# Kernel tuning notes

Hardware: AMD Instinct MI355X
Metric: run time of the kernel (lower is better)

Reference implementation:

```python
import jax, jax.numpy as jnp
import numpy as np

H = 512; W = 512; C = 32; B = 2; N = 120000; HEADS = 2; HD = C // HEADS; S = 9
INDEX_SHIFT = jnp.array([[0,0],[-1,0],[1,0],[0,1],[-1,1],[1,1],[0,-1],[-1,-1],[1,-1]], dtype=jnp.int32)


def setup_inputs() -> dict:
    key = jax.random.key(0)
    ks = jax.random.split(key, 20)
    bev_feats = jax.random.normal(ks[0], (B, N, C), jnp.float32)
    coors = []
    for b in range(B):
        perm = jax.random.permutation(ks[1 + b], H * W)[:N]
        coors.append(jnp.stack([perm // W, perm % W], axis=-1))
    bev_coors = jnp.stack(coors).astype(jnp.int32)
    s = 1.0 / np.sqrt(C)
    u = lambda k, shape, lim: jax.random.uniform(k, shape, jnp.float32, -lim, lim)
    return {
        'bev_feats': bev_feats,
        'bev_coors': bev_coors,
        'ln_w': jnp.ones((C,), jnp.float32),
        'ln_b': jnp.zeros((C,), jnp.float32),
        'wq': u(ks[3], (C, C), s), 'bq': u(ks[4], (C,), s),
        'wk': u(ks[5], (C, C), s), 'bk': u(ks[6], (C,), s),
        'wv': u(ks[7], (C, C), s), 'bv': u(ks[8], (C,), s),
        'pos_w': u(ks[9], (C, 2), 1.0 / np.sqrt(2.0)), 'pos_b': u(ks[10], (C,), 1.0 / np.sqrt(2.0)),
        'in_w': u(ks[11], (3 * C, C), s), 'in_b': jnp.zeros((3 * C,), jnp.float32),
        'out_w': u(ks[12], (C, C), s), 'out_b': jnp.zeros((C,), jnp.float32),
    }


def reference(bev_feats, bev_coors, ln_w, ln_b, wq, bq, wk, bk, wv, bv, pos_w, pos_b, in_w, in_b, out_w, out_b):
    def single(feats, coors):
        # LayerNorm (biased var, eps=1e-5)
        mu = feats.mean(-1, keepdims=True)
        var = feats.var(-1, keepdims=True)
        x = (feats - mu) / jnp.sqrt(var + 1e-5) * ln_w + ln_b
        # qkv 1x1 conv == linear
        q = x @ wq.T + bq
        k = x @ wk.T + bk
        v = x @ wv.T + bv
        # dense grid lookup: coord -> voxel index (-1 if empty)
        flat0 = coors[:, 0] * W + coors[:, 1]
        grid = jnp.full((H * W,), -1, jnp.int32).at[flat0].set(jnp.arange(N, dtype=jnp.int32))
        sc = coors[None] + INDEX_SHIFT[:, None]                      # [9,N,2]
        valid = (sc[..., 0] >= 0) & (sc[..., 0] < H) & (sc[..., 1] >= 0) & (sc[..., 1] < W)
        flat = jnp.clip(sc[..., 0], 0, H - 1) * W + jnp.clip(sc[..., 1], 0, W - 1)
        idx = jnp.where(valid, grid[flat], -1)                       # [9,N]
        pos = INDEX_SHIFT.astype(x.dtype) @ pos_w.T + pos_b          # [9,C]
        m = (idx >= 0)[..., None]
        tv = jnp.where(m, v[idx] + pos[:, None, :], 0.0)             # [9,N,C]
        tk = jnp.where(m, k[idx], 0.0)
        keyt = jnp.swapaxes(tk, 0, 1)                                # [N,9,C]
        valt = jnp.swapaxes(tv, 0, 1)
        # tiny MHA: query len 1, kv len 9, 2 heads (dropout inactive at eval)
        qp = q @ in_w[:C].T + in_b[:C]
        kp = keyt @ in_w[C:2 * C].T + in_b[C:2 * C]
        vp = valt @ in_w[2 * C:].T + in_b[2 * C:]
        qh = qp.reshape(N, HEADS, HD)
        kh = kp.reshape(N, S, HEADS, HD)
        vh = vp.reshape(N, S, HEADS, HD)
        attn = jax.nn.softmax(jnp.einsum('nhd,nshd->nhs', qh, kh) / np.sqrt(HD), axis=-1)
        o = jnp.einsum('nhs,nshd->nhd', attn, vh).reshape(N, C)
        o = o @ out_w.T + out_b
        # scatter to pseudo image [C,H,W]
        canvas = jnp.zeros((C, H * W), o.dtype).at[:, flat0].set(o.T)
        return canvas.reshape(C, H, W)
    return jax.vmap(single)(bev_feats, bev_coors)
```

## Files before the change

kernel.cpp:

```cpp
#include <hip/hip_runtime.h>
#include <hip/hip_fp16.h>
#include <cstdio>
#include <cstdint>

#define HH 512
#define WW 512
#define CC 32
#define BB 2
#define NN 120000
#define HWPIX (HH*WW)
#define NPTS (BB*NN)
#define NPIX (BB*HWPIX)
#define NBLK (NPIX/256)

__device__ __forceinline__ void h8_to_f8(float4 raw, float* o) {
    const __half2* h = (const __half2*)&raw;
    #pragma unroll
    for (int i = 0; i < 4; ++i) {
        float2 f = __half22float2(h[i]);
        o[2 * i] = f.x; o[2 * i + 1] = f.y;
    }
}

__global__ void compose_mats(const float* __restrict__ wq, const float* __restrict__ wk,
                             const float* __restrict__ wv, const float* __restrict__ in_w,
                             const float* __restrict__ out_w, float* __restrict__ M) {
    int tid = blockIdx.x * blockDim.x + threadIdx.x;
    if (tid >= 4096) return;
    int which = tid >> 10;
    int e = tid & 1023;
    int cp = e & 31;
    int j  = e >> 5;
    if (which < 3) {
        const float* w = (which == 0) ? wq : ((which == 1) ? wk : wv);
        const float* Wrow = in_w + (which * 32 + cp) * 32;
        float acc = 0.f;
        #pragma unroll
        for (int t = 0; t < 32; ++t) acc += Wrow[t] * w[t * 32 + j];
        M[which * 1024 + j * 32 + cp] = acc;
    } else {
        M[3 * 1024 + j * 32 + cp] = out_w[cp * 32 + j];
    }
}

__global__ void compose_vecs(const float* __restrict__ bq, const float* __restrict__ bk,
                             const float* __restrict__ bv, const float* __restrict__ in_w,
                             const float* __restrict__ in_b, const float* __restrict__ pos_w,
                             const float* __restrict__ pos_b, float* __restrict__ V) {
    int tid = threadIdx.x;
    if (tid < 32) {
        float a = 0.f, b = 0.f, c = 0.f;
        #pragma unroll
        for (int t = 0; t < 32; ++t) {
            a += in_w[tid * 32 + t] * bq[t];
            b += in_w[(32 + tid) * 32 + t] * bk[t];
            c += in_w[(64 + tid) * 32 + t] * bv[t];
        }
        V[tid]      = a + in_b[tid];
        V[32 + tid] = b;
        V[64 + tid] = c;
    } else if (tid < 128) {
        int grp = (tid - 32) >> 5;
        int cp  = tid & 31;
        float acc = 0.f;
        #pragma unroll
        for (int t = 0; t < 32; ++t) {
            float src = (grp == 0) ? pos_w[t * 2 + 0] : ((grp == 1) ? pos_w[t * 2 + 1] : pos_b[t]);
            acc += in_w[(64 + cp) * 32 + t] * src;
        }
        V[96 + grp * 32 + cp] = acc;
    }
}

__global__ void build_grid(const int* __restrict__ coors, int* __restrict__ grid) {
    int P = blockIdx.x * blockDim.x + threadIdx.x;
    if (P >= NPTS) return;
    int b = P / NN;
    int n = P - b * NN;
    int y = coors[P * 2 + 0];
    int x = coors[P * 2 + 1];
    grid[b * HWPIX + y * WW + x] = n;
}

__global__ __launch_bounds__(256) void count_occ(const int* __restrict__ grid, int* __restrict__ cnt) {
    int tid = threadIdx.x;
    int pix = blockIdx.x * 256 + tid;
    bool occ = grid[pix] >= 0;
    unsigned long long mask = __ballot(occ);
    __shared__ int w[4];
    if ((tid & 63) == 0) w[tid >> 6] = __popcll(mask);
    __syncthreads();
    if (tid == 0) cnt[blockIdx.x] = w[0] + w[1] + w[2] + w[3];
}

__global__ __launch_bounds__(256) void scan2048(const int* __restrict__ cnt, int* __restrict__ off) {
    __shared__ int ps[256];
    int tid = threadIdx.x;
    int v[8], loc[8];
    int t = 0;
    #pragma unroll
    for (int k = 0; k < 8; ++k) { v[k] = cnt[tid * 8 + k]; loc[k] = t; t += v[k]; }
    ps[tid] = t;
    __syncthreads();
    for (int d = 1; d < 256; d <<= 1) {
        int val = ps[tid];
        int add = (tid >= d) ? ps[tid - d] : 0;
        __syncthreads();
        ps[tid] = val + add;
        __syncthreads();
    }
    int excl = (tid > 0) ? ps[tid - 1] : 0;
    #pragma unroll
    for (int k = 0; k < 8; ++k) off[tid * 8 + k] = excl + loc[k];
}

__global__ __launch_bounds__(256) void assign_ranks(const int* __restrict__ off,
                                                    int* __restrict__ grid,
                                                    int* __restrict__ rmap,
                                                    int* __restrict__ plist) {
    __shared__ int woff[4];
    int tid = threadIdx.x;
    int pix = blockIdx.x * 256 + tid;
    int n = grid[pix];
    bool occ = n >= 0;
    unsigned long long mask = __ballot(occ);
    int lane = tid & 63, wvi = tid >> 6;
    if (lane == 0) woff[wvi] = __popcll(mask);
    __syncthreads();
    int pre = 0;
    for (int w = 0; w < wvi; ++w) pre += woff[w];
    if (occ) {
        int r = off[blockIdx.x] + pre + __popcll(mask & ((1ull << lane) - 1ull));
        grid[pix] = r;
        rmap[(pix >> 18) * NN + n] = r;
        plist[r] = pix;
    }
}

__global__ __launch_bounds__(256) void stage1(const float* __restrict__ feats,
                                              const float* __restrict__ ln_w,
                                              const float* __restrict__ ln_b,
                                              const float* __restrict__ M,
                                              const float* __restrict__ V,
                                              const int* __restrict__ rmap,
                                              float* __restrict__ qp,
                                              __half* __restrict__ kvh) {
    int gp = blockIdx.x * 256 + threadIdx.x;
    if (gp >= NPTS) return;
    int r = rmap[gp];

    const float* fr = feats + ((size_t)gp << 5);
    float x[32];
    #pragma unroll
    for (int k = 0; k < 8; ++k) ((float4*)x)[k] = ((const float4*)fr)[k];

    float s1 = 0.f, s2 = 0.f;
    #pragma unroll
    for (int j = 0; j < 32; ++j) { s1 += x[j]; s2 += x[j] * x[j]; }
    float mu   = s1 * (1.f / 32.f);
    float var  = s2 * (1.f / 32.f) - mu * mu;
    float rstd = rsqrtf(var + 1e-5f);
    #pragma unroll
    for (int j = 0; j < 32; ++j) x[j] = (x[j] - mu) * rstd * ln_w[j] + ln_b[j];

    float acc[32];

    #pragma unroll
    for (int c = 0; c < 32; ++c) acc[c] = V[c];
    #pragma unroll
    for (int j = 0; j < 32; ++j) {
        float xv = x[j];
        #pragma unroll
        for (int c = 0; c < 32; ++c) acc[c] += xv * M[j * 32 + c];
    }
    {
        float4* qd = (float4*)(qp + ((size_t)r << 5));
        #pragma unroll
        for (int k = 0; k < 8; ++k) qd[k] = ((float4*)acc)[k];
    }

    __half2 kvbuf[32];

    #pragma unroll
    for (int c = 0; c < 32; ++c) acc[c] = V[32 + c];
    #pragma unroll
    for (int j = 0; j < 32; ++j) {
        float xv = x[j];
        #pragma unroll
        for (int c = 0; c < 32; ++c) acc[c] += xv * M[1024 + j * 32 + c];
    }
    #pragma unroll
    for (int c = 0; c < 16; ++c) kvbuf[c] = __floats2half2_rn(acc[2 * c], acc[2 * c + 1]);

    #pragma unroll
    for (int c = 0; c < 32; ++c) acc[c] = V[64 + c];
    #pragma unroll
    for (int j = 0; j < 32; ++j) {
        float xv = x[j];
        #pragma unroll
        for (int c = 0; c < 32; ++c) acc[c] += xv * M[2048 + j * 32 + c];
    }
    #pragma unroll
    for (int c = 0; c < 16; ++c) kvbuf[16 + c] = __floats2half2_rn(acc[2 * c], acc[2 * c + 1]);

    float4* kd = (float4*)(kvh + ((size_t)r << 6));
    #pragma unroll
    for (int k = 0; k < 8; ++k) kd[k] = ((float4*)kvbuf)[k];
}

__global__ __launch_bounds__(256) void stage2(const int* __restrict__ grid,
                                              const int* __restrict__ plist,
                                              const __half* __restrict__ kvh,
                                              const float* __restrict__ M,
                                              const float* __restrict__ V,
                                              const float* __restrict__ in_b,
                                              const float* __restrict__ out_b,
                                              float* __restrict__ qp) {
    __shared__ float lds[128 * 36];

    int w = (blockIdx.x & 7) * 235 + (blockIdx.x >> 3);
    if (w >= 1875) return;
    int t = w * 256 + threadIdx.x;
    int r = t >> 1, h = t & 1;

    int pix = plist[r];
    int b = pix >> 18;
    int p = pix & (HWPIX - 1);
    int y = p >> 9, x = p & 511;

    const int DYC[9] = {0,-1,1,0,-1,1,0,-1,1};
    const int DXC[9] = {0,0,0,1,1,1,-1,-1,-1};

    float qf[16];
    {
        const float4* q4 = (const float4*)(qp + ((size_t)r << 5) + (h << 4));
        #pragma unroll
        for (int k = 0; k < 4; ++k) ((float4*)qf)[k] = q4[k];
    }
    float ebv = 0.f;
    {
        const float* ib = in_b + 32 + (h << 4);
        #pragma unroll
        for (int i = 0; i < 16; ++i) ebv += qf[i] * ib[i];
    }

    int nr[9];
    #pragma unroll
    for (int s = 0; s < 9; ++s) {
        int sy = y + DYC[s], sx = x + DXC[s];
        nr[s] = (sy >= 0 && sy < HH && sx >= 0 && sx < WW) ? grid[(b << 18) + (sy << 9) + sx] : -1;
    }

    float lg[9];
    #pragma unroll
    for (int s = 0; s < 9; ++s) {
        float d = ebv;
        if (nr[s] >= 0) {
            const float4* kp = (const float4*)(kvh + ((size_t)nr[s] << 6) + (h << 4));
            float kf[16];
            h8_to_f8(kp[0], kf); h8_to_f8(kp[1], kf + 8);
            #pragma unroll
            for (int i = 0; i < 16; ++i) d += qf[i] * kf[i];
        }
        lg[s] = d * 0.25f;
    }
    float m = lg[0];
    #pragma unroll
    for (int s = 1; s < 9; ++s) m = fmaxf(m, lg[s]);
    float l = 0.f;
    #pragma unroll
    for (int s = 0; s < 9; ++s) { lg[s] = __expf(lg[s] - m); l += lg[s]; }

    float o16[16];
    #pragma unroll
    for (int i = 0; i < 16; ++i) o16[i] = 0.f;
    float wdy = 0.f, wdx = 0.f, woc = 0.f;
    #pragma unroll
    for (int s = 0; s < 9; ++s) {
        if (nr[s] >= 0) {
            float wgt = lg[s];
            const float4* vp = (const float4*)(kvh + ((size_t)nr[s] << 6) + 32 + (h << 4));
            float vf[16];
            h8_to_f8(vp[0], vf); h8_to_f8(vp[1], vf + 8);
            #pragma unroll
            for (int i = 0; i < 16; ++i) o16[i] += wgt * vf[i];
            wdy += wgt * (float)DYC[s];
            wdx += wgt * (float)DXC[s];
            woc += wgt;
        }
    }
    float rl = 1.f / l;
    {
        const float* PY = V + 96 + (h << 4);
        const float* PX = V + 128 + (h << 4);
        const float* PB = V + 160 + (h << 4);
        const float* B3 = in_b + 64 + (h << 4);
        #pragma unroll
        for (int i = 0; i < 16; ++i)
            o16[i] = (o16[i] + wdy * PY[i] + wdx * PX[i] + woc * PB[i]) * rl + B3[i];
    }

    float of[32];
    #pragma unroll
    for (int j = 0; j < 16; ++j) {
        float po = __shfl_xor(o16[j], 1, 64);
        of[j]      = h ? po : o16[j];
        of[16 + j] = h ? o16[j] : po;
    }

    float acc[32];
    #pragma unroll
    for (int c = 0; c < 32; ++c) acc[c] = out_b[c];
    #pragma unroll
    for (int j = 0; j < 32; ++j) {
        float vj = of[j];
        #pragma unroll
        for (int c = 0; c < 32; ++c) acc[c] += vj * M[3072 + j * 32 + c];
    }
    float st[16];
    #pragma unroll
    for (int k = 0; k < 16; ++k) st[k] = h ? acc[16 + k] : acc[k];

    int i = threadIdx.x >> 1;
    float* lrow = lds + i * 36 + (h << 4);
    #pragma unroll
    for (int k = 0; k < 4; ++k) ((float4*)lrow)[k] = ((float4*)st)[k];
    __syncthreads();

    float* gbase = qp + (size_t)w * 4096;
    #pragma unroll
    for (int k = 0; k < 4; ++k) {
        int g = k * 1024 + threadIdx.x * 4;
        int ii = g >> 5, inner = g & 31;
        float4 val = *(const float4*)(lds + ii * 36 + inner);
        *(float4*)(gbase + g) = val;
    }
}

__global__ __launch_bounds__(256) void stage3(const int* __restrict__ grid,
                                              const float* __restrict__ obuf,
                                              float* __restrict__ out) {
    int w = (blockIdx.x & 7) * 256 + (blockIdx.x >> 3);
    int t = w * 256 + threadIdx.x;
    int b = t >> 18;
    int p = t & (HWPIX - 1);
    int rk = grid[t];
    float r[32];
    if (rk >= 0) {
        const float4* row = (const float4*)(obuf + ((size_t)rk << 5));
        #pragma unroll
        for (int i = 0; i < 8; ++i) ((float4*)r)[i] = row[i];
    } else {
        #pragma unroll
        for (int i = 0; i < 32; ++i) r[i] = 0.f;
    }
    float* outb = out + (size_t)b * CC * HWPIX + p;
    #pragma unroll
    for (int cc = 0; cc < 32; ++cc) outb[cc * HWPIX] = r[cc];
}

extern "C" void kernel_launch(void* const* d_in, const int* in_sizes, int n_in,
                              void* d_out, int out_size, void* d_ws, size_t ws_size,
                              hipStream_t stream) {
    const float* feats = (const float*)d_in[0];
    const int*   coors = (const int*)d_in[1];
    const float* ln_w  = (const float*)d_in[2];
    const float* ln_b  = (const float*)d_in[3];
    const float* wq    = (const float*)d_in[4];
    const float* bq    = (const float*)d_in[5];
    const float* wk    = (const float*)d_in[6];
    const float* bk    = (const float*)d_in[7];
    const float* wv    = (const float*)d_in[8];
    const float* bv    = (const float*)d_in[9];
    const float* pos_w = (const float*)d_in[10];
    const float* pos_b = (const float*)d_in[11];
    const float* in_w  = (const float*)d_in[12];
    const float* in_b  = (const float*)d_in[13];
    const float* out_w = (const float*)d_in[14];
    const float* out_b = (const float*)d_in[15];

    int*    grid = (int*)d_ws;
    float*  qp   = (float*)d_ws + NPIX;
    __half* kvh  = (__half*)((float*)d_ws + NPIX + (size_t)NPTS * 32);
    float*  M    = (float*)(kvh + (size_t)NPTS * 64);
    float*  V    = M + 4096;
    size_t need = ((size_t)NPIX + (size_t)NPTS * 32 + (size_t)NPTS * 16 + 4096 + 192) * sizeof(float);
    if (ws_size < need) {
        fprintf(stderr, "kernel_launch: ws too small: %zu < %zu\n", ws_size, need);
        return;
    }
    int* cnt   = (int*)d_out + (out_size - 4096);
    int* off   = cnt + 2048;
    int* rmap  = (int*)d_out + (out_size - 4096 - 2 * NPTS);
    int* plist = rmap + NPTS;

    hipMemsetAsync(grid, 0xFF, (size_t)NPIX * sizeof(int), stream);
    compose_mats<<<16, 256, 0, stream>>>(wq, wk, wv, in_w, out_w, M);
    compose_vecs<<<1, 128, 0, stream>>>(bq, bk, bv, in_w, in_b, pos_w, pos_b, V);
    build_grid<<<(NPTS + 255) / 256, 256, 0, stream>>>(coors, grid);
    count_occ<<<NBLK, 256, 0, stream>>>(grid, cnt);
    scan2048<<<1, 256, 0, stream>>>(cnt, off);
    assign_ranks<<<NBLK, 256, 0, stream>>>(off, grid, rmap, plist);
    stage1<<<(NPTS + 255) / 256, 256, 0, stream>>>(feats, ln_w, ln_b, M, V, rmap, qp, kvh);
    stage2<<<1880, 256, 0, stream>>>(grid, plist, kvh, M, V, in_b, out_b, qp);
    stage3<<<NBLK, 256, 0, stream>>>(grid, qp, (float*)d_out);
}
```

Before: 232.7 us.

## Fuse prep kernels, count occupancy via atomics, one-thread-per-point stage2 with fp16 output

Merges compose_mats and compose_vecs into a single prep kernel that also zeroes the per-block counters. The count_occ pass is dropped by having build_grid atomically increment per-256-pixel counts. Stage2 now gives each thread both heads of one point instead of splitting heads across lane pairs, which removes the shuffle at the cost of more registers. Its output goes to a separate fp16 buffer, halving the traffic that stage3 gathers, with some loss of precision.

```diff
diff --git a/kernel.cpp b/kernel.cpp
--- a/kernel.cpp
+++ b/kernel.cpp
@@ -22,75 +22,70 @@
     }
 }
 
-__global__ void compose_mats(const float* __restrict__ wq, const float* __restrict__ wk,
-                             const float* __restrict__ wv, const float* __restrict__ in_w,
-                             const float* __restrict__ out_w, float* __restrict__ M) {
-    int tid = blockIdx.x * blockDim.x + threadIdx.x;
-    if (tid >= 4096) return;
-    int which = tid >> 10;
-    int e = tid & 1023;
-    int cp = e & 31;
-    int j  = e >> 5;
-    if (which < 3) {
-        const float* w = (which == 0) ? wq : ((which == 1) ? wk : wv);
-        const float* Wrow = in_w + (which * 32 + cp) * 32;
-        float acc = 0.f;
-        #pragma unroll
-        for (int t = 0; t < 32; ++t) acc += Wrow[t] * w[t * 32 + j];
-        M[which * 1024 + j * 32 + cp] = acc;
+__global__ __launch_bounds__(256) void prep(const float* __restrict__ wq, const float* __restrict__ wk,
+                          const float* __restrict__ wv, const float* __restrict__ in_w,
+                          const float* __restrict__ out_w,
+                          const float* __restrict__ bq, const float* __restrict__ bk,
+                          const float* __restrict__ bv, const float* __restrict__ in_b,
+                          const float* __restrict__ pos_w, const float* __restrict__ pos_b,
+                          float* __restrict__ M, float* __restrict__ V, int* __restrict__ cnt) {
+    int blk = blockIdx.x;
+    if (blk < 16) {
+        int tid = blk * 256 + threadIdx.x;
+        int which = tid >> 10;
+        int e = tid & 1023;
+        int cp = e & 31;
+        int j  = e >> 5;
+        if (which < 3) {
+            const float* w = (which == 0) ? wq : ((which == 1) ? wk : wv);
+            const float* Wrow = in_w + (which * 32 + cp) * 32;
+            float acc = 0.f;
+            #pragma unroll
+            for (int t = 0; t < 32; ++t) acc += Wrow[t] * w[t * 32 + j];
+            M[which * 1024 + j * 32 + cp] = acc;
+        } else {
+            M[3 * 1024 + j * 32 + cp] = out_w[cp * 32 + j];
+        }
+    } else if (blk == 16) {
+        int tid = threadIdx.x;
+        if (tid < 32) {
+            float a = 0.f, b = 0.f, c = 0.f;
+            #pragma unroll
+            for (int t = 0; t < 32; ++t) {
+                a += in_w[tid * 32 + t] * bq[t];
+                b += in_w[(32 + tid) * 32 + t] * bk[t];
+                c += in_w[(64 + tid) * 32 + t] * bv[t];
+            }
+            V[tid]      = a + in_b[tid];
+            V[32 + tid] = b;
+            V[64 + tid] = c;
+        } else if (tid < 128) {
+            int grp = (tid - 32) >> 5;
+            int cp  = tid & 31;
+            float acc = 0.f;
+            #pragma unroll
+            for (int t = 0; t < 32; ++t) {
+                float src = (grp == 0) ? pos_w[t * 2 + 0] : ((grp == 1) ? pos_w[t * 2 + 1] : pos_b[t]);
+                acc += in_w[(64 + cp) * 32 + t] * src;
+            }
+            V[96 + grp * 32 + cp] = acc;
+        }
     } else {
-        M[3 * 1024 + j * 32 + cp] = out_w[cp * 32 + j];
-    }
-}
-
-__global__ void compose_vecs(const float* __restrict__ bq, const float* __restrict__ bk,
-                             const float* __restrict__ bv, const float* __restrict__ in_w,
-                             const float* __restrict__ in_b, const float* __restrict__ pos_w,
-                             const float* __restrict__ pos_b, float* __restrict__ V) {
-    int tid = threadIdx.x;
-    if (tid < 32) {
-        float a = 0.f, b = 0.f, c = 0.f;
-        #pragma unroll
-        for (int t = 0; t < 32; ++t) {
-            a += in_w[tid * 32 + t] * bq[t];
-            b += in_w[(32 + tid) * 32 + t] * bk[t];
-            c += in_w[(64 + tid) * 32 + t] * bv[t];
-        }
-        V[tid]      = a + in_b[tid];
-        V[32 + tid] = b;
-        V[64 + tid] = c;
-    } else if (tid < 128) {
-        int grp = (tid - 32) >> 5;
-        int cp  = tid & 31;
-        float acc = 0.f;
-        #pragma unroll
-        for (int t = 0; t < 32; ++t) {
-            float src = (grp == 0) ? pos_w[t * 2 + 0] : ((grp == 1) ? pos_w[t * 2 + 1] : pos_b[t]);
-            acc += in_w[(64 + cp) * 32 + t] * src;
-        }
-        V[96 + grp * 32 + cp] = acc;
-    }
-}
-
-__global__ void build_grid(const int* __restrict__ coors, int* __restrict__ grid) {
+        for (int i = threadIdx.x; i < 2048; i += 256) cnt[i] = 0;
+    }
+}
+
+__global__ void build_grid(const int* __restrict__ coors, int* __restrict__ grid,
+                           int* __restrict__ cnt) {
     int P = blockIdx.x * blockDim.x + threadIdx.x;
     if (P >= NPTS) return;
     int b = P / NN;
     int n = P - b * NN;
     int y = coors[P * 2 + 0];
     int x = coors[P * 2 + 1];
-    grid[b * HWPIX + y * WW + x] = n;
-}
-
-__global__ __launch_bounds__(256) void count_occ(const int* __restrict__ grid, int* __restrict__ cnt) {
-    int tid = threadIdx.x;
-    int pix = blockIdx.x * 256 + tid;
-    bool occ = grid[pix] >= 0;
-    unsigned long long mask = __ballot(occ);
-    __shared__ int w[4];
-    if ((tid & 63) == 0) w[tid >> 6] = __popcll(mask);
-    __syncthreads();
-    if (tid == 0) cnt[blockIdx.x] = w[0] + w[1] + w[2] + w[3];
+    int pix = b * HWPIX + y * WW + x;
+    grid[pix] = n;
+    atomicAdd(&cnt[pix >> 8], 1);
 }
 
 __global__ __launch_bounds__(256) void scan2048(const int* __restrict__ cnt, int* __restrict__ off) {
@@ -215,15 +210,18 @@
                                               const float* __restrict__ V,
                                               const float* __restrict__ in_b,
                                               const float* __restrict__ out_b,
-                                              float* __restrict__ qp) {
-    __shared__ float lds[128 * 36];
-
-    int w = (blockIdx.x & 7) * 235 + (blockIdx.x >> 3);
-    if (w >= 1875) return;
-    int t = w * 256 + threadIdx.x;
-    int r = t >> 1, h = t & 1;
-
-    int pix = plist[r];
+                                              const float* __restrict__ qp,
+                                              __half* __restrict__ obuf) {
+    __shared__ float lsf[256 * 18];
+
+    int w = (blockIdx.x & 7) * 118 + (blockIdx.x >> 3);
+    if (w >= 938) return;
+    int tid = threadIdx.x;
+    int r0 = w * 256;
+    int r = r0 + tid;
+    int rc = (r < NPTS) ? r : (NPTS - 1);
+
+    int pix = plist[rc];
     int b = pix >> 18;
     int p = pix & (HWPIX - 1);
     int y = p >> 9, x = p & 511;
@@ -231,17 +229,11 @@
     const int DYC[9] = {0,-1,1,0,-1,1,0,-1,1};
     const int DXC[9] = {0,0,0,1,1,1,-1,-1,-1};
 
-    float qf[16];
+    float qf[32];
     {
-        const float4* q4 = (const float4*)(qp + ((size_t)r << 5) + (h << 4));
-        #pragma unroll
-        for (int k = 0; k < 4; ++k) ((float4*)qf)[k] = q4[k];
-    }
-    float ebv = 0.f;
-    {
-        const float* ib = in_b + 32 + (h << 4);
-        #pragma unroll
-        for (int i = 0; i < 16; ++i) ebv += qf[i] * ib[i];
+        const float4* q4 = (const float4*)(qp + ((size_t)rc << 5));
+        #pragma unroll
+        for (int k = 0; k < 8; ++k) ((float4*)qf)[k] = q4[k];
     }
 
     int nr[9];
@@ -251,94 +243,104 @@
         nr[s] = (sy >= 0 && sy < HH && sx >= 0 && sx < WW) ? grid[(b << 18) + (sy << 9) + sx] : -1;
     }
 
-    float lg[9];
+    float eb0 = 0.f, eb1 = 0.f;
+    #pragma unroll
+    for (int i = 0; i < 16; ++i) {
+        eb0 += qf[i]      * in_b[32 + i];
+        eb1 += qf[16 + i] * in_b[48 + i];
+    }
+
+    float lg0[9], lg1[9];
     #pragma unroll
     for (int s = 0; s < 9; ++s) {
-        float d = ebv;
+        float d0 = eb0, d1 = eb1;
         if (nr[s] >= 0) {
-            const float4* kp = (const float4*)(kvh + ((size_t)nr[s] << 6) + (h << 4));
-            float kf[16];
-            h8_to_f8(kp[0], kf); h8_to_f8(kp[1], kf + 8);
+            const float4* kp = (const float4*)(kvh + ((size_t)nr[s] << 6));
+            float kf[32];
+            h8_to_f8(kp[0], kf);      h8_to_f8(kp[1], kf + 8);
+            h8_to_f8(kp[2], kf + 16); h8_to_f8(kp[3], kf + 24);
             #pragma unroll
-            for (int i = 0; i < 16; ++i) d += qf[i] * kf[i];
+            for (int i = 0; i < 16; ++i) {
+                d0 += qf[i]      * kf[i];
+                d1 += qf[16 + i] * kf[16 + i];
+            }
         }
-        lg[s] = d * 0.25f;
-    }
-    float m = lg[0];
-    #pragma unroll
-    for (int s = 1; s < 9; ++s) m = fmaxf(m, lg[s]);
-    float l = 0.f;
-    #pragma unroll
-    for (int s = 0; s < 9; ++s) { lg[s] = __expf(lg[s] - m); l += lg[s]; }
-
-    float o16[16];
-    #pragma unroll
-    for (int i = 0; i < 16; ++i) o16[i] = 0.f;
-    float wdy = 0.f, wdx = 0.f, woc = 0.f;
+        lg0[s] = d0 * 0.25f;
+        lg1[s] = d1 * 0.25f;
+    }
+    float m0 = lg0[0], m1 = lg1[0];
+    #pragma unroll
+    for (int s = 1; s < 9; ++s) { m0 = fmaxf(m0, lg0[s]); m1 = fmaxf(m1, lg1[s]); }
+    float l0 = 0.f, l1 = 0.f;
+    #pragma unroll
+    for (int s = 0; s < 9; ++s) {
+        lg0[s] = __expf(lg0[s] - m0); l0 += lg0[s];
+        lg1[s] = __expf(lg1[s] - m1); l1 += lg1[s];
+    }
+
+    float o[32];
+    #pragma unroll
+    for (int i = 0; i < 32; ++i) o[i] = 0.f;
+    float wdy0 = 0.f, wdx0 = 0.f, woc0 = 0.f;
+    float wdy1 = 0.f, wdx1 = 0.f, woc1 = 0.f;
     #pragma unroll
     for (int s = 0; s < 9; ++s) {
         if (nr[s] >= 0) {
-            float wgt = lg[s];
-            const float4* vp = (const float4*)(kvh + ((size_t)nr[s] << 6) + 32 + (h << 4));
-            float vf[16];
-            h8_to_f8(vp[0], vf); h8_to_f8(vp[1], vf + 8);
+            float w0 = lg0[s], w1 = lg1[s];
+            const float4* vp = (const float4*)(kvh + ((size_t)nr[s] << 6)) + 4;
+            float vf[32];
+            h8_to_f8(vp[0], vf);      h8_to_f8(vp[1], vf + 8);
+            h8_to_f8(vp[2], vf + 16); h8_to_f8(vp[3], vf + 24);
             #pragma unroll
-            for (int i = 0; i < 16; ++i) o16[i] += wgt * vf[i];
-            wdy += wgt * (float)DYC[s];
-            wdx += wgt * (float)DXC[s];
-            woc += wgt;
+            for (int i = 0; i < 16; ++i) {
+                o[i]      += w0 * vf[i];
+                o[16 + i] += w1 * vf[16 + i];
+            }
+            wdy0 += w0 * (float)DYC[s]; wdx0 += w0 * (float)DXC[s]; woc0 += w0;
+            wdy1 += w1 * (float)DYC[s]; wdx1 += w1 * (float)DXC[s]; woc1 += w1;
         }
     }
-    float rl = 1.f / l;
+    float rl0 = 1.f / l0, rl1 = 1.f / l1;
+    #pragma unroll
+    for (int i = 0; i < 16; ++i) {
+        o[i]      = (o[i]      + wdy0 * V[96 + i]      + wdx0 * V[128 + i]      + woc0 * V[160 + i])      * rl0 + in_b[64 + i];
+        o[16 + i] = (o[16 + i] + wdy1 * V[96 + 16 + i] + wdx1 * V[128 + 16 + i] + woc1 * V[160 + 16 + i]) * rl1 + in_b[80 + i];
+    }
+
+    float acc[32];
+    #pragma unroll
+    for (int c = 0; c < 32; ++c) acc[c] = out_b[c];
+    #pragma unroll
+    for (int j = 0; j < 32; ++j) {
+        float vj = o[j];
+        #pragma unroll
+        for (int c = 0; c < 32; ++c) acc[c] += vj * M[3072 + j * 32 + c];
+    }
+
     {
-        const float* PY = V + 96 + (h << 4);
-        const float* PX = V + 128 + (h << 4);
-        const float* PB = V + 160 + (h << 4);
-        const float* B3 = in_b + 64 + (h << 4);
-        #pragma unroll
-        for (int i = 0; i < 16; ++i)
-            o16[i] = (o16[i] + wdy * PY[i] + wdx * PX[i] + woc * PB[i]) * rl + B3[i];
-    }
-
-    float of[32];
-    #pragma unroll
-    for (int j = 0; j < 16; ++j) {
-        float po = __shfl_xor(o16[j], 1, 64);
-        of[j]      = h ? po : o16[j];
-        of[16 + j] = h ? o16[j] : po;
-    }
-
-    float acc[32];
-    #pragma unroll
-    for (int c = 0; c < 32; ++c) acc[c] = out_b[c];
-    #pragma unroll
-    for (int j = 0; j < 32; ++j) {
-        float vj = of[j];
-        #pragma unroll
-        for (int c = 0; c < 32; ++c) acc[c] += vj * M[3072 + j * 32 + c];
-    }
-    float st[16];
-    #pragma unroll
-    for (int k = 0; k < 16; ++k) st[k] = h ? acc[16 + k] : acc[k];
-
-    int i = threadIdx.x >> 1;
-    float* lrow = lds + i * 36 + (h << 4);
-    #pragma unroll
-    for (int k = 0; k < 4; ++k) ((float4*)lrow)[k] = ((float4*)st)[k];
+        float hbuf[16];
+        __half2* hp = (__half2*)hbuf;
+        #pragma unroll
+        for (int c = 0; c < 16; ++c) hp[c] = __floats2half2_rn(acc[2 * c], acc[2 * c + 1]);
+        float* lrow = lsf + tid * 18;
+        #pragma unroll
+        for (int j = 0; j < 8; ++j) *(float2*)(lrow + j * 2) = ((float2*)hbuf)[j];
+    }
     __syncthreads();
 
-    float* gbase = qp + (size_t)w * 4096;
-    #pragma unroll
-    for (int k = 0; k < 4; ++k) {
-        int g = k * 1024 + threadIdx.x * 4;
-        int ii = g >> 5, inner = g & 31;
-        float4 val = *(const float4*)(lds + ii * 36 + inner);
-        *(float4*)(gbase + g) = val;
+    #pragma unroll
+    for (int k = 0; k < 8; ++k) {
+        int ii  = k * 32 + (tid >> 3);
+        int col = tid & 7;
+        if (r0 + ii < NPTS) {
+            float2 val = *(const float2*)(lsf + ii * 18 + col * 2);
+            *(float2*)(obuf + ((size_t)(r0 + ii) << 5) + col * 4) = val;
+        }
     }
 }
 
 __global__ __launch_bounds__(256) void stage3(const int* __restrict__ grid,
-                                              const float* __restrict__ obuf,
+                                              const __half* __restrict__ obuf,
                                               float* __restrict__ out) {
     int w = (blockIdx.x & 7) * 256 + (blockIdx.x >> 3);
     int t = w * 256 + threadIdx.x;
@@ -348,8 +350,8 @@
     float r[32];
     if (rk >= 0) {
         const float4* row = (const float4*)(obuf + ((size_t)rk << 5));
-        #pragma unroll
-        for (int i = 0; i < 8; ++i) ((float4*)r)[i] = row[i];
+        float4 raw0 = row[0], raw1 = row[1], raw2 = row[2], raw3 = row[3];
+        h8_to_f8(raw0, r); h8_to_f8(raw1, r + 8); h8_to_f8(raw2, r + 16); h8_to_f8(raw3, r + 24);
     } else {
         #pragma unroll
         for (int i = 0; i < 32; ++i) r[i] = 0.f;
@@ -381,10 +383,12 @@
 
     int*    grid = (int*)d_ws;
     float*  qp   = (float*)d_ws + NPIX;
-    __half* kvh  = (__half*)((float*)d_ws + NPIX + (size_t)NPTS * 32);
-    float*  M    = (float*)(kvh + (size_t)NPTS * 64);
+    __half* kvh  = (__half*)(qp + (size_t)NPTS * 32);
+    __half* obuf = kvh + (size_t)NPTS * 64;
+    float*  M    = (float*)(obuf + (size_t)NPTS * 32);
     float*  V    = M + 4096;
-    size_t need = ((size_t)NPIX + (size_t)NPTS * 32 + (size_t)NPTS * 16 + 4096 + 192) * sizeof(float);
+    size_t need = ((size_t)NPIX + (size_t)NPTS * 32 + (size_t)NPTS * 16
+                   + (size_t)NPTS * 8 + 4096 + 192) * sizeof(float);
     if (ws_size < need) {
         fprintf(stderr, "kernel_launch: ws too small: %zu < %zu\n", ws_size, need);
         return;
@@ -395,13 +399,11 @@
     int* plist = rmap + NPTS;
 
     hipMemsetAsync(grid, 0xFF, (size_t)NPIX * sizeof(int), stream);
-    compose_mats<<<16, 256, 0, stream>>>(wq, wk, wv, in_w, out_w, M);
-    compose_vecs<<<1, 128, 0, stream>>>(bq, bk, bv, in_w, in_b, pos_w, pos_b, V);
-    build_grid<<<(NPTS + 255) / 256, 256, 0, stream>>>(coors, grid);
-    count_occ<<<NBLK, 256, 0, stream>>>(grid, cnt);
+    prep<<<18, 256, 0, stream>>>(wq, wk, wv, in_w, out_w, bq, bk, bv, in_b, pos_w, pos_b, M, V, cnt);
+    build_grid<<<(NPTS + 255) / 256, 256, 0, stream>>>(coors, grid, cnt);
     scan2048<<<1, 256, 0, stream>>>(cnt, off);
     assign_ranks<<<NBLK, 256, 0, stream>>>(off, grid, rmap, plist);
     stage1<<<(NPTS + 255) / 256, 256, 0, stream>>>(feats, ln_w, ln_b, M, V, rmap, qp, kvh);
-    stage2<<<1880, 256, 0, stream>>>(grid, plist, kvh, M, V, in_b, out_b, qp);
-    stage3<<<NBLK, 256, 0, stream>>>(grid, qp, (float*)d_out);
-}
+    stage2<<<944, 256, 0, stream>>>(grid, plist, kvh, M, V, in_b, out_b, qp, obuf);
+    stage3<<<NBLK, 256, 0, stream>>>(grid, obuf, (float*)d_out);
+}
```

Result: no change. 236.8 us (+1.8%).
